# Optimization experiments

Measured on AMD Instinct MI355X. Metric: run time of the kernel, lower is better.

Reference implementation:

```python
import jax, jax.numpy as jnp
import numpy as np

EMBED_DIM = 1024
NUM_HEADS = 16
HEAD_DIM = EMBED_DIM // NUM_HEADS
B, T = 2, 2048


def setup_inputs() -> dict:
    key = jax.random.key(0)
    ks = jax.random.split(key, 5)
    s_in = 1.0 / np.sqrt(EMBED_DIM)
    return {
        "x": jax.random.normal(ks[0], (B, T, EMBED_DIM), dtype=jnp.float32),
        "qkv_w": jax.random.uniform(ks[1], (3 * EMBED_DIM, EMBED_DIM), jnp.float32, -s_in, s_in),
        "qkv_b": jax.random.uniform(ks[2], (3 * EMBED_DIM,), jnp.float32, -s_in, s_in),
        "out_w": jax.random.uniform(ks[3], (EMBED_DIM, EMBED_DIM), jnp.float32, -s_in, s_in),
        "out_b": jax.random.uniform(ks[4], (EMBED_DIM,), jnp.float32, -s_in, s_in),
    }


def reference(x, qkv_w, qkv_b, out_w, out_b):
    b, t, d = x.shape
    scale = HEAD_DIM ** -0.5
    # fused qkv projection: (B, T, 3D)
    qkv = jnp.einsum("btd,ed->bte", x, qkv_w) + qkv_b
    qkv = qkv.reshape(b, t, 3, NUM_HEADS, HEAD_DIM)
    q, k, v = jnp.moveaxis(qkv, 2, 0)  # each (B, T, H, Dh)
    # scores: (B, H, T, T)
    scores = jnp.einsum("bqhd,bkhd->bhqk", q, k) * scale
    attn = jax.nn.softmax(scores, axis=-1)
    # attention output: (B, T, H, Dh) -> (B, T, D)
    ctx = jnp.einsum("bhqk,bkhd->bqhd", attn, v).reshape(b, t, d)
    return jnp.einsum("btd,ed->bte", ctx, out_w) + out_b
```

## Files before the change

kernel.cpp:

```cpp
#include <hip/hip_runtime.h>

typedef __bf16 bf16;
typedef __bf16 bf16x4 __attribute__((ext_vector_type(4)));
typedef __bf16 bf16x8 __attribute__((ext_vector_type(8)));
typedef float f32x4 __attribute__((ext_vector_type(4)));

#define MFMA16(a, b, c) __builtin_amdgcn_mfma_f32_16x16x32_bf16(a, b, c, 0, 0, 0)

__device__ __forceinline__ void lds_load16(void* lds, const void* g) {
  __builtin_amdgcn_global_load_lds(
      (const __attribute__((address_space(1))) unsigned int*)g,
      (__attribute__((address_space(3))) unsigned int*)lds, 16, 0, 0);
}

__global__ void cvt3(const float* __restrict__ x, const float* __restrict__ qw,
                     const float* __restrict__ ow, bf16* __restrict__ xb,
                     bf16* __restrict__ qwb, bf16* __restrict__ owb) {
  const int i = blockIdx.x * blockDim.x + threadIdx.x;
  const float* src;
  bf16* dst;
  int k;
  if (i < 1048576) {
    src = x; dst = xb; k = i;
  } else if (i < 1048576 + 786432) {
    src = qw; dst = qwb; k = i - 1048576;
  } else {
    src = ow; dst = owb; k = i - (1048576 + 786432);
  }
  const float4 v = ((const float4*)src)[k];
  bf16x4 o;
  o[0] = (bf16)v.x; o[1] = (bf16)v.y; o[2] = (bf16)v.z; o[3] = (bf16)v.w;
  ((bf16x4*)dst)[k] = o;
}

template <int MODE>
__global__ __launch_bounds__(256, 2) void gemm_bt(
    const bf16* __restrict__ A, const bf16* __restrict__ B,
    const float* __restrict__ bias, float* __restrict__ Cf,
    bf16* __restrict__ Qb, bf16* __restrict__ KF, bf16* __restrict__ VF,
    int N, int K) {
  __shared__ bf16 As[128][64];
  __shared__ bf16 Bs[128][64];
  const int tid = threadIdx.x;
  const int w = tid >> 6, lane = tid & 63;
  const int l15 = lane & 15, quad = lane >> 4;
  const int lr = lane >> 3;
  const int lc = (lane & 7) * 8;
  const int bn = blockIdx.x, bm = blockIdx.y;
  const int wm = (w >> 1) * 64, wn = (w & 1) * 64;

  const bf16* Abase = A + (size_t)(bm * 128) * K;
  const bf16* Bbase = B + (size_t)(bn * 128) * K;

  f32x4 acc[4][4] = {};

  for (int k0 = 0; k0 < K; k0 += 64) {
#pragma unroll
    for (int c = 0; c < 4; ++c) {
      const int row = w * 32 + c * 8;
      lds_load16(&As[row][0], Abase + (size_t)(row + lr) * K + k0 + lc);
      lds_load16(&Bs[row][0], Bbase + (size_t)(row + lr) * K + k0 + lc);
    }
    __syncthreads();
#pragma unroll
    for (int kk = 0; kk < 64; kk += 32) {
      bf16x8 am[4], bnf[4];
#pragma unroll
      for (int i = 0; i < 4; ++i)
        am[i] = *(const bf16x8*)&As[wm + i * 16 + l15][kk + quad * 8];
#pragma unroll
      for (int j = 0; j < 4; ++j)
        bnf[j] = *(const bf16x8*)&Bs[wn + j * 16 + l15][kk + quad * 8];
#pragma unroll
      for (int i = 0; i < 4; ++i)
#pragma unroll
        for (int j = 0; j < 4; ++j)
          acc[i][j] = MFMA16(am[i], bnf[j], acc[i][j]);
    }
    __syncthreads();
  }

#pragma unroll
  for (int j = 0; j < 4; ++j) {
    const int gcol = bn * 128 + wn + j * 16 + l15;
    const float bv = bias[gcol];
#pragma unroll
    for (int i = 0; i < 4; ++i) {
      const int t0 = bm * 128 + wm + i * 16 + quad * 4;
      if (MODE == 0) {
#pragma unroll
        for (int r = 0; r < 4; ++r)
          Cf[(size_t)(t0 + r) * N + gcol] = acc[i][j][r] + bv;
      } else if (gcol < 1024) {
#pragma unroll
        for (int r = 0; r < 4; ++r)
          Qb[(size_t)(t0 + r) * 1024 + gcol] =
              (bf16)((acc[i][j][r] + bv) * 0.18033688f);
      } else if (gcol < 2048) {
        const int dhl = gcol - 1024;
        const int hh = dhl >> 6, dh = dhl & 63;
        const int tl = t0 & 2047, bb = t0 >> 11;
        const size_t frag = ((size_t)(bb * 16 + hh) * 32 + (tl >> 6)) * 8 +
                            ((tl & 63) >> 4) * 2 + (dh >> 5);
        bf16* p = &KF[frag * 512 +
                      (size_t)(((dh >> 3) & 3) * 16 + (tl & 15)) * 8 + (dh & 7)];
#pragma unroll
        for (int r = 0; r < 4; ++r) p[r * 8] = (bf16)(acc[i][j][r] + bv);
      } else {
        const int dhl = gcol - 2048;
        const int hh = dhl >> 6, dh = dhl & 63;
        const int tl = t0 & 2047, bb = t0 >> 11;
        const size_t frag = ((size_t)(bb * 16 + hh) * 32 + (tl >> 6)) * 8 +
                            (dh >> 4) * 2 + ((tl & 63) >> 5);
        bf16x4 pv;
#pragma unroll
        for (int r = 0; r < 4; ++r) pv[r] = (bf16)(acc[i][j][r] + bv);
        *(bf16x4*)&VF[frag * 512 +
                      (size_t)(((tl & 31) >> 3) * 16 + (dh & 15)) * 8 +
                      (tl & 7)] = pv;
      }
    }
  }
}

__global__ __launch_bounds__(256, 2) void attn(const bf16* __restrict__ Qb,
                                               const bf16* __restrict__ KF,
                                               const bf16* __restrict__ VF,
                                               bf16* __restrict__ CTX) {
  __shared__ bf16 Ps[128][72];
  const int tid = threadIdx.x, w = tid >> 6, lane = tid & 63;
  const int l15 = lane & 15, quad = lane >> 4;
  const int blk = blockIdx.x;
  const int qt = blk & 15, h = (blk >> 4) & 15, b = blk >> 8;
  const int q0 = qt * 128;

  const bf16* qrow0 =
      Qb + (size_t)(b * 2048 + q0 + w * 32 + l15) * 1024 + h * 64;
  const bf16* qrow1 = qrow0 + (size_t)16 * 1024;
  const bf16x8 bq0a = *(const bf16x8*)&qrow0[quad * 8];
  const bf16x8 bq0b = *(const bf16x8*)&qrow0[32 + quad * 8];
  const bf16x8 bq1a = *(const bf16x8*)&qrow1[quad * 8];
  const bf16x8 bq1b = *(const bf16x8*)&qrow1[32 + quad * 8];

  const bf16* kfb = KF + (size_t)(b * 16 + h) * 131072 + (size_t)lane * 8;
  const bf16* vfb = VF + (size_t)(b * 16 + h) * 131072 + (size_t)lane * 8;

  bf16x8 kf[2][4], vf[2][4];
#pragma unroll
  for (int j = 0; j < 4; ++j)
#pragma unroll
    for (int k2 = 0; k2 < 2; ++k2) {
      kf[k2][j] = *(const bf16x8*)&kfb[(j * 2 + k2) << 9];
      vf[k2][j] = *(const bf16x8*)&vfb[(j * 2 + k2) << 9];
    }

  float l_run[2] = {0.f, 0.f};
  f32x4 o[2][4] = {};

  for (int kt6 = 0; kt6 < 32; ++kt6) {
    f32x4 s[2][4] = {};
#pragma unroll
    for (int k2 = 0; k2 < 2; ++k2)
#pragma unroll
      for (int j = 0; j < 4; ++j) {
        s[0][j] = MFMA16(kf[k2][j], k2 ? bq0b : bq0a, s[0][j]);
        s[1][j] = MFMA16(kf[k2][j], k2 ? bq1b : bq1a, s[1][j]);
      }

    {
      const bf16* kn = kfb + ((size_t)(kt6 + 1) << 12);
#pragma unroll
      for (int j = 0; j < 4; ++j)
#pragma unroll
        for (int k2 = 0; k2 < 2; ++k2)
          kf[k2][j] = *(const bf16x8*)&kn[(j * 2 + k2) << 9];
    }

#pragma unroll
    for (int i = 0; i < 2; ++i) {
      float sum = 0.f;
#pragma unroll
      for (int j = 0; j < 4; ++j) {
        bf16x4 pk;
#pragma unroll
        for (int r = 0; r < 4; ++r) {
          const float p = __builtin_amdgcn_exp2f(s[i][j][r]);
          sum += p;
          pk[r] = (bf16)p;
        }
        *(bf16x4*)&Ps[w * 32 + i * 16 + l15][j * 16 + quad * 4] = pk;
      }
      l_run[i] += sum;
    }

#pragma unroll
    for (int k2 = 0; k2 < 2; ++k2) {
      const bf16x8 bp0 = *(const bf16x8*)&Ps[w * 32 + l15][k2 * 32 + quad * 8];
      const bf16x8 bp1 =
          *(const bf16x8*)&Ps[w * 32 + 16 + l15][k2 * 32 + quad * 8];
#pragma unroll
      for (int j = 0; j < 4; ++j) {
        o[0][j] = MFMA16(vf[k2][j], bp0, o[0][j]);
        o[1][j] = MFMA16(vf[k2][j], bp1, o[1][j]);
      }
    }

    {
      const bf16* vn = vfb + ((size_t)(kt6 + 1) << 12);
#pragma unroll
      for (int j = 0; j < 4; ++j)
#pragma unroll
        for (int k2 = 0; k2 < 2; ++k2)
          vf[k2][j] = *(const bf16x8*)&vn[(j * 2 + k2) << 9];
    }
  }

#pragma unroll
  for (int i = 0; i < 2; ++i) {
    l_run[i] += __shfl_xor(l_run[i], 16);
    l_run[i] += __shfl_xor(l_run[i], 32);
  }

#pragma unroll
  for (int i = 0; i < 2; ++i) {
    const float inv = 1.f / l_run[i];
    bf16* crow =
        CTX + (size_t)(b * 2048 + q0 + w * 32 + i * 16 + l15) * 1024 + h * 64;
#pragma unroll
    for (int j = 0; j < 4; ++j) {
      bf16x4 ov;
#pragma unroll
      for (int r = 0; r < 4; ++r) ov[r] = (bf16)(o[i][j][r] * inv);
      *(bf16x4*)&crow[j * 16 + quad * 4] = ov;
    }
  }
}

extern "C" void kernel_launch(void* const* d_in, const int* in_sizes, int n_in,
                              void* d_out, int out_size, void* d_ws,
                              size_t ws_size, hipStream_t stream) {
  const float* x = (const float*)d_in[0];
  const float* qkv_w = (const float*)d_in[1];
  const float* qkv_b = (const float*)d_in[2];
  const float* out_w = (const float*)d_in[3];
  const float* out_b = (const float*)d_in[4];
  float* out = (float*)d_out;

  bf16* xb = (bf16*)d_ws;
  bf16* wqkv = xb + (size_t)4096 * 1024;
  bf16* wout = wqkv + (size_t)3072 * 1024;
  bf16* qb = wout + (size_t)1024 * 1024;
  bf16* kf = qb + (size_t)4096 * 1024;
  bf16* vf = kf + (size_t)4096 * 1024;
  bf16* ctx = vf + (size_t)4096 * 1024;

  cvt3<<<2097152 / 256, 256, 0, stream>>>(x, qkv_w, out_w, xb, wqkv, wout);

  gemm_bt<1><<<dim3(24, 32), 256, 0, stream>>>(xb, wqkv, qkv_b, nullptr, qb,
                                               kf, vf, 3072, 1024);
  attn<<<512, 256, 0, stream>>>(qb, kf, vf, ctx);
  gemm_bt<0><<<dim3(8, 32), 256, 0, stream>>>(ctx, wout, out_b, out, nullptr,
                                              nullptr, nullptr, 1024, 1024);
}
```

Measured before the change: 196.7 us.

## Split attention keys across waves and retile output GEMM for more blocks

The attention kernel now assigns 32 query rows per block and gives each of the four waves a quarter of the key range. Partial outputs and row sums are reduced through shared memory before normalisation, which quadruples the grid. The output projection uses 64-row tiles so twice as many blocks launch, and the QKV GEMM is de-templated. This aims to fill more CUs, at the cost of an extra LDS reduction and reloading Q per smaller block.

After: 287.3 us. 46.0% more time.

```diff
diff --git a/kernel.cpp b/kernel.cpp
--- a/kernel.cpp
+++ b/kernel.cpp
@@ -33,12 +33,11 @@
   ((bf16x4*)dst)[k] = o;
 }
 
-template <int MODE>
-__global__ __launch_bounds__(256, 2) void gemm_bt(
+__global__ __launch_bounds__(256, 2) void gemm_qkv(
     const bf16* __restrict__ A, const bf16* __restrict__ B,
-    const float* __restrict__ bias, float* __restrict__ Cf,
-    bf16* __restrict__ Qb, bf16* __restrict__ KF, bf16* __restrict__ VF,
-    int N, int K) {
+    const float* __restrict__ bias, bf16* __restrict__ Qb,
+    bf16* __restrict__ KF, bf16* __restrict__ VF) {
+  const int K = 1024;
   __shared__ bf16 As[128][64];
   __shared__ bf16 Bs[128][64];
   const int tid = threadIdx.x;
@@ -87,11 +86,7 @@
 #pragma unroll
     for (int i = 0; i < 4; ++i) {
       const int t0 = bm * 128 + wm + i * 16 + quad * 4;
-      if (MODE == 0) {
-#pragma unroll
-        for (int r = 0; r < 4; ++r)
-          Cf[(size_t)(t0 + r) * N + gcol] = acc[i][j][r] + bv;
-      } else if (gcol < 1024) {
+      if (gcol < 1024) {
 #pragma unroll
         for (int r = 0; r < 4; ++r)
           Qb[(size_t)(t0 + r) * 1024 + gcol] =
@@ -123,27 +118,92 @@
   }
 }
 
+__global__ __launch_bounds__(256, 2) void gemm_out(
+    const bf16* __restrict__ A, const bf16* __restrict__ B,
+    const float* __restrict__ bias, float* __restrict__ Cf) {
+  __shared__ bf16 As[64][64];
+  __shared__ bf16 Bs[128][64];
+  const int tid = threadIdx.x;
+  const int w = tid >> 6, lane = tid & 63;
+  const int l15 = lane & 15, quad = lane >> 4;
+  const int lr = lane >> 3, lc = (lane & 7) * 8;
+  const int bn = blockIdx.x, bm = blockIdx.y;
+
+  const bf16* Abase = A + (size_t)(bm * 64) * 1024;
+  const bf16* Bbase = B + (size_t)(bn * 128) * 1024;
+
+  f32x4 acc[4][2] = {};
+
+  for (int k0 = 0; k0 < 1024; k0 += 64) {
+#pragma unroll
+    for (int c = 0; c < 2; ++c) {
+      const int row = w * 16 + c * 8;
+      lds_load16(&As[row][0], Abase + (size_t)(row + lr) * 1024 + k0 + lc);
+    }
+#pragma unroll
+    for (int c = 0; c < 4; ++c) {
+      const int row = w * 32 + c * 8;
+      lds_load16(&Bs[row][0], Bbase + (size_t)(row + lr) * 1024 + k0 + lc);
+    }
+    __syncthreads();
+#pragma unroll
+    for (int kk = 0; kk < 64; kk += 32) {
+      bf16x8 am[4], bnf[2];
+#pragma unroll
+      for (int i = 0; i < 4; ++i)
+        am[i] = *(const bf16x8*)&As[i * 16 + l15][kk + quad * 8];
+#pragma unroll
+      for (int j = 0; j < 2; ++j)
+        bnf[j] = *(const bf16x8*)&Bs[w * 32 + j * 16 + l15][kk + quad * 8];
+#pragma unroll
+      for (int i = 0; i < 4; ++i)
+#pragma unroll
+        for (int j = 0; j < 2; ++j)
+          acc[i][j] = MFMA16(am[i], bnf[j], acc[i][j]);
+    }
+    __syncthreads();
+  }
+
+#pragma unroll
+  for (int j = 0; j < 2; ++j) {
+    const int gcol = bn * 128 + w * 32 + j * 16 + l15;
+    const float bv = bias[gcol];
+#pragma unroll
+    for (int i = 0; i < 4; ++i)
+#pragma unroll
+      for (int r = 0; r < 4; ++r) {
+        const int grow = bm * 64 + i * 16 + quad * 4 + r;
+        Cf[(size_t)grow * 1024 + gcol] = acc[i][j][r] + bv;
+      }
+  }
+}
+
 __global__ __launch_bounds__(256, 2) void attn(const bf16* __restrict__ Qb,
                                                const bf16* __restrict__ KF,
                                                const bf16* __restrict__ VF,
                                                bf16* __restrict__ CTX) {
-  __shared__ bf16 Ps[128][72];
+  __shared__ __align__(16) char smem[26624];
+  bf16(*Ps)[72] = (bf16(*)[72])smem;
+  float* Or = (float*)smem;
+  float* Lr = (float*)(smem + 24576);
+
   const int tid = threadIdx.x, w = tid >> 6, lane = tid & 63;
   const int l15 = lane & 15, quad = lane >> 4;
   const int blk = blockIdx.x;
-  const int qt = blk & 15, h = (blk >> 4) & 15, b = blk >> 8;
-  const int q0 = qt * 128;
-
-  const bf16* qrow0 =
-      Qb + (size_t)(b * 2048 + q0 + w * 32 + l15) * 1024 + h * 64;
+  const int qt = blk & 63, h = (blk >> 6) & 15, b = blk >> 10;
+  const int q0 = qt * 32;
+
+  const bf16* qrow0 = Qb + (size_t)(b * 2048 + q0 + l15) * 1024 + h * 64;
   const bf16* qrow1 = qrow0 + (size_t)16 * 1024;
   const bf16x8 bq0a = *(const bf16x8*)&qrow0[quad * 8];
   const bf16x8 bq0b = *(const bf16x8*)&qrow0[32 + quad * 8];
   const bf16x8 bq1a = *(const bf16x8*)&qrow1[quad * 8];
   const bf16x8 bq1b = *(const bf16x8*)&qrow1[32 + quad * 8];
 
-  const bf16* kfb = KF + (size_t)(b * 16 + h) * 131072 + (size_t)lane * 8;
-  const bf16* vfb = VF + (size_t)(b * 16 + h) * 131072 + (size_t)lane * 8;
+  const bf16* kfb =
+      KF + (size_t)(b * 16 + h) * 131072 + ((size_t)w << 15) + (size_t)lane * 8;
+  const bf16* vfb =
+      VF + (size_t)(b * 16 + h) * 131072 + ((size_t)w << 15) + (size_t)lane * 8;
 
   bf16x8 kf[2][4], vf[2][4];
 #pragma unroll
@@ -157,7 +217,7 @@
   float l_run[2] = {0.f, 0.f};
   f32x4 o[2][4] = {};
 
-  for (int kt6 = 0; kt6 < 32; ++kt6) {
+  for (int t = 0; t < 8; ++t) {
     f32x4 s[2][4] = {};
 #pragma unroll
     for (int k2 = 0; k2 < 2; ++k2)
@@ -168,7 +228,7 @@
       }
 
     {
-      const bf16* kn = kfb + ((size_t)(kt6 + 1) << 12);
+      const bf16* kn = kfb + ((size_t)(t + 1) << 12);
 #pragma unroll
       for (int j = 0; j < 4; ++j)
 #pragma unroll
@@ -206,7 +266,7 @@
     }
 
     {
-      const bf16* vn = vfb + ((size_t)(kt6 + 1) << 12);
+      const bf16* vn = vfb + ((size_t)(t + 1) << 12);
 #pragma unroll
       for (int j = 0; j < 4; ++j)
 #pragma unroll
@@ -215,6 +275,36 @@
     }
   }
 
+  __syncthreads();
+#pragma unroll
+  for (int j = 0; j < 4; ++j) {
+    if (j == w) continue;
+    const int jj = (j > w) ? j - 1 : j;
+#pragma unroll
+    for (int i = 0; i < 2; ++i)
+      *(f32x4*)&Or[(((w * 3 + jj) * 2 + i) * 64 + lane) * 4] = o[i][j];
+  }
+  Lr[(w * 2 + 0) * 64 + lane] = l_run[0];
+  Lr[(w * 2 + 1) * 64 + lane] = l_run[1];
+  __syncthreads();
+
+  f32x4 oc[2];
+#pragma unroll
+  for (int i = 0; i < 2; ++i)
+    oc[i] = (w == 0) ? o[i][0] : (w == 1) ? o[i][1] : (w == 2) ? o[i][2]
+                                                              : o[i][3];
+#pragma unroll
+  for (int ww = 0; ww < 4; ++ww) {
+    if (ww == w) continue;
+    const int jj2 = (w > ww) ? w - 1 : w;
+#pragma unroll
+    for (int i = 0; i < 2; ++i) {
+      const f32x4 tv = *(const f32x4*)&Or[(((ww * 3 + jj2) * 2 + i) * 64 + lane) * 4];
+#pragma unroll
+      for (int r = 0; r < 4; ++r) oc[i][r] += tv[r];
+      l_run[i] += Lr[(ww * 2 + i) * 64 + lane];
+    }
+  }
 #pragma unroll
   for (int i = 0; i < 2; ++i) {
     l_run[i] += __shfl_xor(l_run[i], 16);
@@ -224,15 +314,11 @@
 #pragma unroll
   for (int i = 0; i < 2; ++i) {
     const float inv = 1.f / l_run[i];
-    bf16* crow =
-        CTX + (size_t)(b * 2048 + q0 + w * 32 + i * 16 + l15) * 1024 + h * 64;
-#pragma unroll
-    for (int j = 0; j < 4; ++j) {
-      bf16x4 ov;
-#pragma unroll
-      for (int r = 0; r < 4; ++r) ov[r] = (bf16)(o[i][j][r] * inv);
-      *(bf16x4*)&crow[j * 16 + quad * 4] = ov;
-    }
+    bf16x4 ov;
+#pragma unroll
+    for (int r = 0; r < 4; ++r) ov[r] = (bf16)(oc[i][r] * inv);
+    *(bf16x4*)&CTX[(size_t)(b * 2048 + q0 + i * 16 + l15) * 1024 + h * 64 +
+                   w * 16 + quad * 4] = ov;
   }
 }
 
@@ -256,9 +342,7 @@
 
   cvt3<<<2097152 / 256, 256, 0, stream>>>(x, qkv_w, out_w, xb, wqkv, wout);
 
-  gemm_bt<1><<<dim3(24, 32), 256, 0, stream>>>(xb, wqkv, qkv_b, nullptr, qb,
-                                               kf, vf, 3072, 1024);
-  attn<<<512, 256, 0, stream>>>(qb, kf, vf, ctx);
-  gemm_bt<0><<<dim3(8, 32), 256, 0, stream>>>(ctx, wout, out_b, out, nullptr,
-                                              nullptr, nullptr, 1024, 1024);
-}
+  gemm_qkv<<<dim3(24, 32), 256, 0, stream>>>(xb, wqkv, qkv_b, qb, kf, vf);
+  attn<<<2048, 256, 0, stream>>>(qb, kf, vf, ctx);
+  gemm_out<<<dim3(8, 64), 256, 0, stream>>>(ctx, wout, out_b, out);
+}
```
